# Kernel optimization log

Hardware: AMD Instinct MI355X
Metric: run time of the kernel (lower is better)

## Reference

```python
import jax, jax.numpy as jnp
import numpy as np

D_MODEL = 512
N = 2048
BS = 8


def setup_inputs() -> dict:
    key = jax.random.key(0)
    ks = jax.random.split(key, 5)
    inputs1 = jax.random.normal(ks[0], (BS, N, D_MODEL), dtype=jnp.float32)
    inputs2 = jax.random.normal(ks[1], (BS, N, D_MODEL), dtype=jnp.float32)
    # torch Linear weights: init.normal_(std=0.001), bias=0
    Wq = 0.001 * jax.random.normal(ks[2], (D_MODEL, D_MODEL), dtype=jnp.float32)
    Wk = 0.001 * jax.random.normal(ks[3], (D_MODEL, D_MODEL), dtype=jnp.float32)
    Wv = 0.001 * jax.random.normal(ks[4], (D_MODEL, D_MODEL), dtype=jnp.float32)
    bq = jnp.zeros((D_MODEL,), dtype=jnp.float32)
    bk = jnp.zeros((D_MODEL,), dtype=jnp.float32)
    bv = jnp.zeros((D_MODEL,), dtype=jnp.float32)
    # nn.Parameter(torch.ones((n, n)))
    position_biases = jnp.ones((N, N), dtype=jnp.float32)
    return {"inputs1": inputs1, "inputs2": inputs2, "Wq": Wq, "bq": bq,
            "Wk": Wk, "bk": bk, "Wv": Wv, "bv": bv,
            "position_biases": position_biases}


def reference(inputs1, inputs2, Wq, bq, Wk, bk, Wv, bv, position_biases):
    # torch Linear: y = x @ W.T + b
    q = inputs1 @ Wq.T + bq                     # [b, n, d]
    k = inputs1 @ Wk.T + bk                     # [b, s, d]
    v = inputs2 @ Wv.T + bv                     # [b, s, d]
    # exp(k[b,s,d] + bias[t,s]) = exp(bias)[t,s] * exp(k)[b,s,d] -> separable,
    # avoiding the original's (n, bs, n, dim) broadcast intermediate.
    expB = jnp.exp(position_biases)             # [t, s]
    ek = jnp.exp(k)                             # [b, s, d]
    num = jnp.einsum('ts,bsd->btd', expB, ek * v)
    den = jnp.einsum('ts,bsd->btd', expB, ek)
    return jax.nn.sigmoid(q) * (num / den)      # [b, n, d]
```

## Files before the change

### kernel.cpp

```cpp
#include <hip/hip_runtime.h>

typedef float  f32x4  __attribute__((ext_vector_type(4)));
typedef __bf16 bf16x8 __attribute__((ext_vector_type(8)));
typedef __bf16 bf16x4 __attribute__((ext_vector_type(4)));
typedef __bf16 bf16x2 __attribute__((ext_vector_type(2)));

#define D_MODEL 512
#define SEQ     2048
#define BATCH   8
#define ROWS    (BATCH * SEQ)

#define ASYNC_COPY16(dst_lds, src_glb)                                          \
  __builtin_amdgcn_global_load_lds(                                             \
      (const __attribute__((address_space(1))) void*)(src_glb),                 \
      (__attribute__((address_space(3))) void*)(dst_lds), 16, 0, 0)

__global__ void cvt_x_kernel(const float* __restrict__ in0,
                             const float* __restrict__ in1,
                             __bf16* __restrict__ o0, __bf16* __restrict__ o1,
                             int n4) {
  const float* in = blockIdx.y ? in1 : in0;
  __bf16* out = blockIdx.y ? o1 : o0;
  int i = blockIdx.x * 256 + threadIdx.x;
  if (i >= n4) return;
  float4 v = ((const float4*)in)[i];
  bf16x4 o = { (__bf16)v.x, (__bf16)v.y, (__bf16)v.z, (__bf16)v.w };
  ((bf16x4*)out)[i] = o;
}

__global__ void cvt_w_kernel(const float* __restrict__ Wq,
                             const float* __restrict__ Wk,
                             const float* __restrict__ Wv,
                             const float* __restrict__ bq,
                             const float* __restrict__ bk,
                             __bf16* __restrict__ wqk, __bf16* __restrict__ wvb,
                             float* __restrict__ bqk, int n4) {
  const int y = blockIdx.y;
  const float* in = (y == 0) ? Wq : (y == 1) ? Wk : Wv;
  __bf16* out = (y == 0) ? wqk : (y == 1) ? (wqk + n4 * 4) : wvb;
  int i = blockIdx.x * 256 + threadIdx.x;
  if (y < 2 && blockIdx.x == 0 && threadIdx.x < D_MODEL) {
    int t = threadIdx.x;
    bqk[y * D_MODEL + t] = (y == 0) ? bq[t] : bk[t];
  }
  if (i >= n4) return;
  float4 v = ((const float4*)in)[i];
  bf16x4 o = { (__bf16)v.x, (__bf16)v.y, (__bf16)v.z, (__bf16)v.w };
  ((bf16x4*)out)[i] = o;
}

__global__ void exp_bf16x4_kernel(const float* __restrict__ in,
                                  __bf16* __restrict__ out, int n4) {
  int i = blockIdx.x * 256 + threadIdx.x;
  if (i >= n4) return;
  float4 v = ((const float4*)in)[i];
  bf16x4 o = { (__bf16)__expf(v.x), (__bf16)__expf(v.y),
               (__bf16)__expf(v.z), (__bf16)__expf(v.w) };
  ((bf16x4*)out)[i] = o;
}


template<int DUAL>
__global__ __launch_bounds__(256) void gemm_bk64_kernel(
    const __bf16* __restrict__ A, const __bf16* __restrict__ Bt,
    const float* __restrict__ bias,
    __bf16* __restrict__ out0, __bf16* __restrict__ out1, int K)
{
  __shared__ __align__(16) __bf16 As[128 * 64];
  __shared__ __align__(16) __bf16 Bs[128 * 64];

  const int tid  = threadIdx.x;
  const int wave = tid >> 6;
  const int lane = tid & 63;
  const int quad = lane >> 4;
  const int l16  = lane & 15;
  const int wm   = (wave >> 1) * 64;
  const int wn   = (wave & 1) * 64;
  const int m0 = blockIdx.x * 128;
  const int n0 = blockIdx.y * 128;
  const int l8r = lane >> 3;
  const int scol = ((lane & 7) ^ l8r) * 8;

  const __bf16* ga[4]; const __bf16* gb[4];
  __bf16* la[4]; __bf16* lb[4];
  #pragma unroll
  for (int i = 0; i < 4; ++i) {
    ga[i] = A  + (long long)(m0 + i * 32 + wave * 8 + l8r) * K + scol;
    gb[i] = Bt + (long long)(n0 + i * 32 + wave * 8 + l8r) * K + scol;
    la[i] = As + (i * 32 + wave * 8) * 64;
    lb[i] = Bs + (i * 32 + wave * 8) * 64;
  }

  f32x4 acc[4][4];
  #pragma unroll
  for (int i = 0; i < 4; ++i)
    #pragma unroll
    for (int j = 0; j < 4; ++j) acc[i][j] = (f32x4){0.f, 0.f, 0.f, 0.f};

  for (int k0 = 0; k0 < K; k0 += 64) {
    #pragma unroll
    for (int i = 0; i < 4; ++i) {
      ASYNC_COPY16(la[i], ga[i] + k0);
      ASYNC_COPY16(lb[i], gb[i] + k0);
    }
    __syncthreads();

    #pragma unroll
    for (int kk = 0; kk < 2; ++kk) {
      const int slot = ((quad + kk * 4) ^ (l16 & 7)) * 8;
      bf16x8 af[4], bfr[4];
      #pragma unroll
      for (int i = 0; i < 4; ++i)
        af[i] = *(const bf16x8*)&As[(wm + i * 16 + l16) * 64 + slot];
      #pragma unroll
      for (int j = 0; j < 4; ++j)
        bfr[j] = *(const bf16x8*)&Bs[(wn + j * 16 + l16) * 64 + slot];
      #pragma unroll
      for (int i = 0; i < 4; ++i)
        #pragma unroll
        for (int j = 0; j < 4; ++j)
          acc[i][j] = __builtin_amdgcn_mfma_f32_16x16x32_bf16(af[i], bfr[j],
                                                              acc[i][j], 0, 0, 0);
    }
    __syncthreads();
  }

  #pragma unroll
  for (int j = 0; j < 4; ++j) {
    const int col = n0 + wn + j * 16 + l16;
    const float bv = bias[col];
    #pragma unroll
    for (int i = 0; i < 4; ++i) {
      #pragma unroll
      for (int r = 0; r < 4; ++r) {
        const int row = m0 + wm + i * 16 + quad * 4 + r;
        float x = acc[i][j][r] + bv;
        if (DUAL) {
          if (col < D_MODEL) {
            out0[(long long)row * D_MODEL + col] = (__bf16)(1.f / (1.f + __expf(-x)));
          } else {
            out1[(long long)row * D_MODEL + (col - D_MODEL)] = (__bf16)x;
          }
        } else {
          out0[(long long)row * D_MODEL + col] = (__bf16)x;
        }
      }
    }
  }
}

__global__ __launch_bounds__(256) void einsum_fused_kernel(
    const __bf16* __restrict__ A, const __bf16* __restrict__ BtAll,
    const __bf16* __restrict__ sigq, float* __restrict__ out)
{
  __shared__ __align__(16) __bf16 As[128 * 64];
  __shared__ __align__(16) __bf16 Bs[128 * 64];

  const int b = blockIdx.z;
  const __bf16* Bt = BtAll + (long long)b * (2 * D_MODEL) * SEQ;
  const int K = SEQ;

  const int tid  = threadIdx.x;
  const int wave = tid >> 6;
  const int lane = tid & 63;
  const int quad = lane >> 4;
  const int l16  = lane & 15;
  const int wm   = (wave >> 1) * 64;
  const int wn   = (wave & 1) * 64;
  const int m0 = blockIdx.x * 128;
  const int n0 = blockIdx.y * 128;
  const int l8r = lane >> 3;
  const int scol = ((lane & 7) ^ l8r) * 8;

  const __bf16* ga[4]; const __bf16* gb[4];
  __bf16* la[4]; __bf16* lb[4];
  #pragma unroll
  for (int i = 0; i < 4; ++i) {
    ga[i] = A  + (long long)(m0 + i * 32 + wave * 8 + l8r) * K + scol;
    gb[i] = Bt + (long long)(n0 + i * 32 + wave * 8 + l8r) * K + scol;
    la[i] = As + (i * 32 + wave * 8) * 64;
    lb[i] = Bs + (i * 32 + wave * 8) * 64;
  }

  f32x4 acc[4][4];
  #pragma unroll
  for (int i = 0; i < 4; ++i)
    #pragma unroll
    for (int j = 0; j < 4; ++j) acc[i][j] = (f32x4){0.f, 0.f, 0.f, 0.f};

  for (int k0 = 0; k0 < K; k0 += 64) {
    #pragma unroll
    for (int i = 0; i < 4; ++i) {
      ASYNC_COPY16(la[i], ga[i] + k0);
      ASYNC_COPY16(lb[i], gb[i] + k0);
    }
    __syncthreads();

    #pragma unroll
    for (int kk = 0; kk < 2; ++kk) {
      const int slot = ((quad + kk * 4) ^ (l16 & 7)) * 8;
      bf16x8 af[4], bfr[4];
      #pragma unroll
      for (int i = 0; i < 4; ++i)
        af[i] = *(const bf16x8*)&As[(wm + i * 16 + l16) * 64 + slot];
      #pragma unroll
      for (int j = 0; j < 4; ++j)
        bfr[j] = *(const bf16x8*)&Bs[(wn + j * 16 + l16) * 64 + slot];
      #pragma unroll
      for (int i = 0; i < 4; ++i)
        #pragma unroll
        for (int j = 0; j < 4; ++j)
          acc[i][j] = __builtin_amdgcn_mfma_f32_16x16x32_bf16(af[i], bfr[j],
                                                              acc[i][j], 0, 0, 0);
    }
    __syncthreads();
  }

  const int g = (n0 + wn) >> 6;
  #pragma unroll
  for (int j = 0; j < 2; ++j) {
    const int d = g * 32 + j * 16 + l16;
    #pragma unroll
    for (int i = 0; i < 4; ++i) {
      #pragma unroll
      for (int r = 0; r < 4; ++r) {
        const int row = m0 + wm + i * 16 + quad * 4 + r;
        const long long off = ((long long)b * SEQ + row) * D_MODEL + d;
        const float num = acc[i][j][r];
        const float den = acc[i][j + 2][r];
        out[off] = (float)sigq[off] * (num / den);
      }
    }
  }
}

__global__ __launch_bounds__(256) void transform_transpose_kernel(
    const __bf16* __restrict__ kb, const __bf16* __restrict__ vb,
    __bf16* __restrict__ ekvT)
{
  __shared__ float t_ekv[64][67];
  __shared__ float t_ek[64][67];
  const int b  = blockIdx.z;
  const int s0 = blockIdx.x * 64;
  const int d0 = blockIdx.y * 64;
  const int tx = threadIdx.x;
  const int ty = threadIdx.y;
  const __bf16* kp = kb + (long long)b * SEQ * D_MODEL;
  const __bf16* vp = vb + (long long)b * SEQ * D_MODEL;

  #pragma unroll
  for (int it = 0; it < 8; ++it) {
    const int sl = ty + it * 8;
    const long long base = (long long)(s0 + sl) * D_MODEL + d0 + 2 * tx;
    bf16x2 kk2 = *(const bf16x2*)(kp + base);
    bf16x2 vv2 = *(const bf16x2*)(vp + base);
    float e0 = __expf((float)kk2[0]);
    float e1 = __expf((float)kk2[1]);
    t_ek[sl][2 * tx]      = e0;
    t_ek[sl][2 * tx + 1]  = e1;
    t_ekv[sl][2 * tx]     = e0 * (float)vv2[0];
    t_ekv[sl][2 * tx + 1] = e1 * (float)vv2[1];
  }
  __syncthreads();

  __bf16* outp = ekvT + (long long)b * (2 * D_MODEL) * SEQ;
  #pragma unroll
  for (int it = 0; it < 8; ++it) {
    const int dl = ty + it * 8;
    const int d  = d0 + dl;
    const int gr = (d >> 5) * 64 + (d & 31);
    bf16x2 ev = { (__bf16)t_ekv[2 * tx][dl], (__bf16)t_ekv[2 * tx + 1][dl] };
    bf16x2 ee = { (__bf16)t_ek[2 * tx][dl],  (__bf16)t_ek[2 * tx + 1][dl] };
    *(bf16x2*)(outp + (long long)gr * SEQ + s0 + 2 * tx)        = ev;
    *(bf16x2*)(outp + (long long)(gr + 32) * SEQ + s0 + 2 * tx) = ee;
  }
}

extern "C" void kernel_launch(void* const* d_in, const int* in_sizes, int n_in,
                              void* d_out, int out_size, void* d_ws, size_t ws_size,
                              hipStream_t stream) {
  const float* inputs1 = (const float*)d_in[0];
  const float* inputs2 = (const float*)d_in[1];
  const float* Wq = (const float*)d_in[2];
  const float* bq = (const float*)d_in[3];
  const float* Wk = (const float*)d_in[4];
  const float* bk = (const float*)d_in[5];
  const float* Wv = (const float*)d_in[6];
  const float* bv = (const float*)d_in[7];
  const float* posb = (const float*)d_in[8];
  float* out = (float*)d_out;

  char* ws = (char*)d_ws;
  const long long szX  = (long long)ROWS * D_MODEL * 2;
  const long long szW  = (long long)D_MODEL * D_MODEL * 2;
  const long long szEB = (long long)SEQ * SEQ * 2;
  const long long szT  = (long long)BATCH * 2 * D_MODEL * SEQ * 2;
  __bf16* x1b   = (__bf16*)(ws);                 ws += szX;
  __bf16* x2b   = (__bf16*)(ws);                 ws += szX;
  __bf16* wqk   = (__bf16*)(ws);                 ws += 2 * szW;
  __bf16* wvb   = (__bf16*)(ws);                 ws += szW;
  float*  bqk   = (float*)(ws);                  ws += 2 * D_MODEL * 4;
  __bf16* expBb = (__bf16*)(ws);                 ws += szEB;
  __bf16* sigq  = (__bf16*)(ws);                 ws += szX;
  __bf16* kb2   = (__bf16*)(ws);                 ws += szX;
  __bf16* vb2   = (__bf16*)(ws);                 ws += szX;
  __bf16* ekvT  = (__bf16*)(ws);                 ws += szT;

  const int nX  = ROWS * D_MODEL;
  const int nW  = D_MODEL * D_MODEL;
  const int nEB = SEQ * SEQ;

  {
    dim3 g(nX / 4 / 256, 2, 1);
    cvt_x_kernel<<<g, 256, 0, stream>>>(inputs1, inputs2, x1b, x2b, nX / 4);
  }
  {
    dim3 g(nW / 4 / 256, 3, 1);
    cvt_w_kernel<<<g, 256, 0, stream>>>(Wq, Wk, Wv, bq, bk, wqk, wvb, bqk, nW / 4);
  }
  exp_bf16x4_kernel<<<nEB / 4 / 256, 256, 0, stream>>>(posb, expBb, nEB / 4);

  {
    dim3 gqk(ROWS / 128, (2 * D_MODEL) / 128, 1);
    gemm_bk64_kernel<1><<<gqk, 256, 0, stream>>>(x1b, wqk, bqk, sigq, kb2, D_MODEL);
    dim3 gv(ROWS / 128, D_MODEL / 128, 1);
    gemm_bk64_kernel<0><<<gv, 256, 0, stream>>>(x2b, wvb, bv, vb2, nullptr, D_MODEL);
  }

  {
    dim3 g(SEQ / 64, D_MODEL / 64, BATCH);
    dim3 blk(32, 8, 1);
    transform_transpose_kernel<<<g, blk, 0, stream>>>(kb2, vb2, ekvT);
  }

  {
    dim3 g(SEQ / 128, (2 * D_MODEL) / 128, BATCH);
    einsum_fused_kernel<<<g, 256, 0, stream>>>(expBb, ekvT, sigq, out);
  }
}
```

Measured before the change: 277.1 us.

## Fuse K/V projections with exp-transform and transpose; merge conversion kernels

The three conversion kernels become a single launch. The Q/K/V GEMMs become one projection kernel. Its z=1 half computes K and V tiles together and applies exp(k) and exp(k)*v in the epilogue. It then transposes the result through swizzled LDS straight into the ekvT layout. This removes the separate transform/transpose kernel and the kb/vb round trip through global memory, at the cost of 64KB of LDS and doubled accumulators per block, which may lower occupancy.

```diff
diff --git a/kernel.cpp b/kernel.cpp
--- a/kernel.cpp
+++ b/kernel.cpp
@@ -3,7 +3,6 @@
 typedef float  f32x4  __attribute__((ext_vector_type(4)));
 typedef __bf16 bf16x8 __attribute__((ext_vector_type(8)));
 typedef __bf16 bf16x4 __attribute__((ext_vector_type(4)));
-typedef __bf16 bf16x2 __attribute__((ext_vector_type(2)));
 
 #define D_MODEL 512
 #define SEQ     2048
@@ -15,59 +14,53 @@
       (const __attribute__((address_space(1))) void*)(src_glb),                 \
       (__attribute__((address_space(3))) void*)(dst_lds), 16, 0, 0)
 
-__global__ void cvt_x_kernel(const float* __restrict__ in0,
-                             const float* __restrict__ in1,
-                             __bf16* __restrict__ o0, __bf16* __restrict__ o1,
-                             int n4) {
-  const float* in = blockIdx.y ? in1 : in0;
-  __bf16* out = blockIdx.y ? o1 : o0;
-  int i = blockIdx.x * 256 + threadIdx.x;
-  if (i >= n4) return;
-  float4 v = ((const float4*)in)[i];
-  bf16x4 o = { (__bf16)v.x, (__bf16)v.y, (__bf16)v.z, (__bf16)v.w };
-  ((bf16x4*)out)[i] = o;
+__global__ void cvt_all_kernel(const float* __restrict__ x1,
+                               const float* __restrict__ x2,
+                               const float* __restrict__ posb,
+                               const float* __restrict__ Wq,
+                               const float* __restrict__ Wk,
+                               const float* __restrict__ Wv,
+                               __bf16* __restrict__ x1b, __bf16* __restrict__ x2b,
+                               __bf16* __restrict__ expBb, __bf16* __restrict__ wb)
+{
+  const int y = blockIdx.y;
+  const int i = blockIdx.x * 256 + threadIdx.x;
+  if (y == 0) {
+    float4 v = ((const float4*)x1)[i];
+    bf16x4 o = { (__bf16)v.x, (__bf16)v.y, (__bf16)v.z, (__bf16)v.w };
+    ((bf16x4*)x1b)[i] = o;
+  } else if (y == 1) {
+    float4 v = ((const float4*)x2)[i];
+    bf16x4 o = { (__bf16)v.x, (__bf16)v.y, (__bf16)v.z, (__bf16)v.w };
+    ((bf16x4*)x2b)[i] = o;
+  } else if (y == 2) {
+    if (i < SEQ * SEQ / 4) {
+      float4 v = ((const float4*)posb)[i];
+      bf16x4 o = { (__bf16)__expf(v.x), (__bf16)__expf(v.y),
+                   (__bf16)__expf(v.z), (__bf16)__expf(v.w) };
+      ((bf16x4*)expBb)[i] = o;
+    }
+  } else {
+    const int nW4 = D_MODEL * D_MODEL / 4;
+    if (i < 3 * nW4) {
+      const float* src = (i < nW4) ? Wq : (i < 2 * nW4) ? Wk : Wv;
+      const int ii = i - ((i < nW4) ? 0 : (i < 2 * nW4) ? nW4 : 2 * nW4);
+      float4 v = ((const float4*)src)[ii];
+      bf16x4 o = { (__bf16)v.x, (__bf16)v.y, (__bf16)v.z, (__bf16)v.w };
+      ((bf16x4*)wb)[i] = o;
+    }
+  }
 }
 
-__global__ void cvt_w_kernel(const float* __restrict__ Wq,
-                             const float* __restrict__ Wk,
-                             const float* __restrict__ Wv,
-                             const float* __restrict__ bq,
-                             const float* __restrict__ bk,
-                             __bf16* __restrict__ wqk, __bf16* __restrict__ wvb,
-                             float* __restrict__ bqk, int n4) {
-  const int y = blockIdx.y;
-  const float* in = (y == 0) ? Wq : (y == 1) ? Wk : Wv;
-  __bf16* out = (y == 0) ? wqk : (y == 1) ? (wqk + n4 * 4) : wvb;
-  int i = blockIdx.x * 256 + threadIdx.x;
-  if (y < 2 && blockIdx.x == 0 && threadIdx.x < D_MODEL) {
-    int t = threadIdx.x;
-    bqk[y * D_MODEL + t] = (y == 0) ? bq[t] : bk[t];
-  }
-  if (i >= n4) return;
-  float4 v = ((const float4*)in)[i];
-  bf16x4 o = { (__bf16)v.x, (__bf16)v.y, (__bf16)v.z, (__bf16)v.w };
-  ((bf16x4*)out)[i] = o;
-}
-
-__global__ void exp_bf16x4_kernel(const float* __restrict__ in,
-                                  __bf16* __restrict__ out, int n4) {
-  int i = blockIdx.x * 256 + threadIdx.x;
-  if (i >= n4) return;
-  float4 v = ((const float4*)in)[i];
-  bf16x4 o = { (__bf16)__expf(v.x), (__bf16)__expf(v.y),
-               (__bf16)__expf(v.z), (__bf16)__expf(v.w) };
-  ((bf16x4*)out)[i] = o;
-}
-
-
-template<int DUAL>
-__global__ __launch_bounds__(256) void gemm_bk64_kernel(
-    const __bf16* __restrict__ A, const __bf16* __restrict__ Bt,
-    const float* __restrict__ bias,
-    __bf16* __restrict__ out0, __bf16* __restrict__ out1, int K)
+__global__ __launch_bounds__(256) void proj_kernel(
+    const __bf16* __restrict__ x1b, const __bf16* __restrict__ x2b,
+    const __bf16* __restrict__ wqb, const __bf16* __restrict__ wkb,
+    const __bf16* __restrict__ wvb,
+    const float* __restrict__ bq, const float* __restrict__ bk,
+    const float* __restrict__ bv,
+    __bf16* __restrict__ sigq, __bf16* __restrict__ ekvT)
 {
-  __shared__ __align__(16) __bf16 As[128 * 64];
-  __shared__ __align__(16) __bf16 Bs[128 * 64];
+  __shared__ __align__(16) __bf16 S[4][128 * 64];
 
   const int tid  = threadIdx.x;
   const int wave = tid >> 6;
@@ -80,71 +73,166 @@
   const int n0 = blockIdx.y * 128;
   const int l8r = lane >> 3;
   const int scol = ((lane & 7) ^ l8r) * 8;
-
-  const __bf16* ga[4]; const __bf16* gb[4];
-  __bf16* la[4]; __bf16* lb[4];
-  #pragma unroll
-  for (int i = 0; i < 4; ++i) {
-    ga[i] = A  + (long long)(m0 + i * 32 + wave * 8 + l8r) * K + scol;
-    gb[i] = Bt + (long long)(n0 + i * 32 + wave * 8 + l8r) * K + scol;
-    la[i] = As + (i * 32 + wave * 8) * 64;
-    lb[i] = Bs + (i * 32 + wave * 8) * 64;
-  }
-
-  f32x4 acc[4][4];
-  #pragma unroll
-  for (int i = 0; i < 4; ++i)
-    #pragma unroll
-    for (int j = 0; j < 4; ++j) acc[i][j] = (f32x4){0.f, 0.f, 0.f, 0.f};
-
-  for (int k0 = 0; k0 < K; k0 += 64) {
+  const int K = D_MODEL;
+
+  if (blockIdx.z == 0) {
+    __bf16* As = S[0];
+    __bf16* Bs = S[1];
+    const __bf16* ga[4]; const __bf16* gb[4];
+    __bf16* la[4]; __bf16* lb[4];
     #pragma unroll
     for (int i = 0; i < 4; ++i) {
-      ASYNC_COPY16(la[i], ga[i] + k0);
-      ASYNC_COPY16(lb[i], gb[i] + k0);
+      ga[i] = x1b + (long long)(m0 + i * 32 + wave * 8 + l8r) * K + scol;
+      gb[i] = wqb + (long long)(n0 + i * 32 + wave * 8 + l8r) * K + scol;
+      la[i] = As + (i * 32 + wave * 8) * 64;
+      lb[i] = Bs + (i * 32 + wave * 8) * 64;
+    }
+    f32x4 acc[4][4];
+    #pragma unroll
+    for (int i = 0; i < 4; ++i)
+      #pragma unroll
+      for (int j = 0; j < 4; ++j) acc[i][j] = (f32x4){0.f, 0.f, 0.f, 0.f};
+
+    for (int k0 = 0; k0 < K; k0 += 64) {
+      #pragma unroll
+      for (int i = 0; i < 4; ++i) {
+        ASYNC_COPY16(la[i], ga[i] + k0);
+        ASYNC_COPY16(lb[i], gb[i] + k0);
+      }
+      __syncthreads();
+      #pragma unroll
+      for (int kk = 0; kk < 2; ++kk) {
+        const int slot = ((quad + kk * 4) ^ (l16 & 7)) * 8;
+        bf16x8 af[4], bfr[4];
+        #pragma unroll
+        for (int i = 0; i < 4; ++i)
+          af[i] = *(const bf16x8*)&As[(wm + i * 16 + l16) * 64 + slot];
+        #pragma unroll
+        for (int j = 0; j < 4; ++j)
+          bfr[j] = *(const bf16x8*)&Bs[(wn + j * 16 + l16) * 64 + slot];
+        #pragma unroll
+        for (int i = 0; i < 4; ++i)
+          #pragma unroll
+          for (int j = 0; j < 4; ++j)
+            acc[i][j] = __builtin_amdgcn_mfma_f32_16x16x32_bf16(af[i], bfr[j],
+                                                                acc[i][j], 0, 0, 0);
+      }
+      __syncthreads();
+    }
+    #pragma unroll
+    for (int j = 0; j < 4; ++j) {
+      const int col = n0 + wn + j * 16 + l16;
+      const float bqv = bq[col];
+      #pragma unroll
+      for (int i = 0; i < 4; ++i)
+        #pragma unroll
+        for (int r = 0; r < 4; ++r) {
+          const int row = m0 + wm + i * 16 + quad * 4 + r;
+          float x = acc[i][j][r] + bqv;
+          sigq[(long long)row * D_MODEL + col] = (__bf16)(1.f / (1.f + __expf(-x)));
+        }
+    }
+  } else {
+    __bf16* A1s = S[0];
+    __bf16* A2s = S[1];
+    __bf16* Bks = S[2];
+    __bf16* Bvs = S[3];
+    const __bf16* ga1[4]; const __bf16* ga2[4];
+    const __bf16* gbk[4]; const __bf16* gbv[4];
+    #pragma unroll
+    for (int i = 0; i < 4; ++i) {
+      const long long roff = (long long)(i * 32 + wave * 8 + l8r);
+      ga1[i] = x1b + (m0 + roff) * K + scol;
+      ga2[i] = x2b + (m0 + roff) * K + scol;
+      gbk[i] = wkb + (n0 + roff) * K + scol;
+      gbv[i] = wvb + (n0 + roff) * K + scol;
+    }
+    f32x4 acck[4][4], accv[4][4];
+    #pragma unroll
+    for (int i = 0; i < 4; ++i)
+      #pragma unroll
+      for (int j = 0; j < 4; ++j) {
+        acck[i][j] = (f32x4){0.f, 0.f, 0.f, 0.f};
+        accv[i][j] = (f32x4){0.f, 0.f, 0.f, 0.f};
+      }
+
+    for (int k0 = 0; k0 < K; k0 += 64) {
+      #pragma unroll
+      for (int i = 0; i < 4; ++i) {
+        const int lo = (i * 32 + wave * 8) * 64;
+        ASYNC_COPY16(A1s + lo, ga1[i] + k0);
+        ASYNC_COPY16(A2s + lo, ga2[i] + k0);
+        ASYNC_COPY16(Bks + lo, gbk[i] + k0);
+        ASYNC_COPY16(Bvs + lo, gbv[i] + k0);
+      }
+      __syncthreads();
+      #pragma unroll
+      for (int kk = 0; kk < 2; ++kk) {
+        const int slot = ((quad + kk * 4) ^ (l16 & 7)) * 8;
+        bf16x8 af[4], bfr[4];
+        #pragma unroll
+        for (int i = 0; i < 4; ++i)
+          af[i] = *(const bf16x8*)&A1s[(wm + i * 16 + l16) * 64 + slot];
+        #pragma unroll
+        for (int j = 0; j < 4; ++j)
+          bfr[j] = *(const bf16x8*)&Bks[(wn + j * 16 + l16) * 64 + slot];
+        #pragma unroll
+        for (int i = 0; i < 4; ++i)
+          #pragma unroll
+          for (int j = 0; j < 4; ++j)
+            acck[i][j] = __builtin_amdgcn_mfma_f32_16x16x32_bf16(af[i], bfr[j],
+                                                                 acck[i][j], 0, 0, 0);
+        #pragma unroll
+        for (int i = 0; i < 4; ++i)
+          af[i] = *(const bf16x8*)&A2s[(wm + i * 16 + l16) * 64 + slot];
+        #pragma unroll
+        for (int j = 0; j < 4; ++j)
+          bfr[j] = *(const bf16x8*)&Bvs[(wn + j * 16 + l16) * 64 + slot];
+        #pragma unroll
+        for (int i = 0; i < 4; ++i)
+          #pragma unroll
+          for (int j = 0; j < 4; ++j)
+            accv[i][j] = __builtin_amdgcn_mfma_f32_16x16x32_bf16(af[i], bfr[j],
+                                                                 accv[i][j], 0, 0, 0);
+      }
+      __syncthreads();
+    }
+
+    __bf16* L = &S[0][0];
+    #pragma unroll
+    for (int j = 0; j < 4; ++j) {
+      const int col = wn + j * 16 + l16;
+      const float bkv = bk[n0 + col];
+      const float bvv = bv[n0 + col];
+      const int Rekv = (col >> 5) * 64 + (col & 31);
+      const int Rek  = Rekv + 32;
+      #pragma unroll
+      for (int i = 0; i < 4; ++i) {
+        const int sb = wm + i * 16 + quad * 4;
+        bf16x4 pk, pv;
+        #pragma unroll
+        for (int r = 0; r < 4; ++r) {
+          const float ek = __expf(acck[i][j][r] + bkv);
+          const float vv = accv[i][j][r] + bvv;
+          pk[r] = (__bf16)ek;
+          pv[r] = (__bf16)(ek * vv);
+        }
+        const int c = sb >> 3, w8 = sb & 7;
+        *(bf16x4*)&L[Rekv * 128 + (((c) ^ (Rekv & 15)) << 3) + w8] = pv;
+        *(bf16x4*)&L[Rek  * 128 + (((c) ^ (Rek  & 15)) << 3) + w8] = pk;
+      }
     }
     __syncthreads();
 
-    #pragma unroll
-    for (int kk = 0; kk < 2; ++kk) {
-      const int slot = ((quad + kk * 4) ^ (l16 & 7)) * 8;
-      bf16x8 af[4], bfr[4];
-      #pragma unroll
-      for (int i = 0; i < 4; ++i)
-        af[i] = *(const bf16x8*)&As[(wm + i * 16 + l16) * 64 + slot];
-      #pragma unroll
-      for (int j = 0; j < 4; ++j)
-        bfr[j] = *(const bf16x8*)&Bs[(wn + j * 16 + l16) * 64 + slot];
-      #pragma unroll
-      for (int i = 0; i < 4; ++i)
-        #pragma unroll
-        for (int j = 0; j < 4; ++j)
-          acc[i][j] = __builtin_amdgcn_mfma_f32_16x16x32_bf16(af[i], bfr[j],
-                                                              acc[i][j], 0, 0, 0);
-    }
-    __syncthreads();
-  }
-
-  #pragma unroll
-  for (int j = 0; j < 4; ++j) {
-    const int col = n0 + wn + j * 16 + l16;
-    const float bv = bias[col];
-    #pragma unroll
-    for (int i = 0; i < 4; ++i) {
-      #pragma unroll
-      for (int r = 0; r < 4; ++r) {
-        const int row = m0 + wm + i * 16 + quad * 4 + r;
-        float x = acc[i][j][r] + bv;
-        if (DUAL) {
-          if (col < D_MODEL) {
-            out0[(long long)row * D_MODEL + col] = (__bf16)(1.f / (1.f + __expf(-x)));
-          } else {
-            out1[(long long)row * D_MODEL + (col - D_MODEL)] = (__bf16)x;
-          }
-        } else {
-          out0[(long long)row * D_MODEL + col] = (__bf16)x;
-        }
-      }
+    const long long obase = (long long)(m0 >> 11) * (2 * D_MODEL) * SEQ
+                          + (long long)(m0 & (SEQ - 1));
+    #pragma unroll
+    for (int ii = 0; ii < 16; ++ii) {
+      const int flat = ii * 256 + tid;
+      const int R = flat >> 4;
+      const int c = flat & 15;
+      bf16x8 vv = *(const bf16x8*)&L[R * 128 + ((c ^ (R & 15)) << 3)];
+      *(bf16x8*)(ekvT + obase + (long long)(blockIdx.y * 256 + R) * SEQ + c * 8) = vv;
     }
   }
 }
@@ -231,48 +319,6 @@
         out[off] = (float)sigq[off] * (num / den);
       }
     }
-  }
-}
-
-__global__ __launch_bounds__(256) void transform_transpose_kernel(
-    const __bf16* __restrict__ kb, const __bf16* __restrict__ vb,
-    __bf16* __restrict__ ekvT)
-{
-  __shared__ float t_ekv[64][67];
-  __shared__ float t_ek[64][67];
-  const int b  = blockIdx.z;
-  const int s0 = blockIdx.x * 64;
-  const int d0 = blockIdx.y * 64;
-  const int tx = threadIdx.x;
-  const int ty = threadIdx.y;
-  const __bf16* kp = kb + (long long)b * SEQ * D_MODEL;
-  const __bf16* vp = vb + (long long)b * SEQ * D_MODEL;
-
-  #pragma unroll
-  for (int it = 0; it < 8; ++it) {
-    const int sl = ty + it * 8;
-    const long long base = (long long)(s0 + sl) * D_MODEL + d0 + 2 * tx;
-    bf16x2 kk2 = *(const bf16x2*)(kp + base);
-    bf16x2 vv2 = *(const bf16x2*)(vp + base);
-    float e0 = __expf((float)kk2[0]);
-    float e1 = __expf((float)kk2[1]);
-    t_ek[sl][2 * tx]      = e0;
-    t_ek[sl][2 * tx + 1]  = e1;
-    t_ekv[sl][2 * tx]     = e0 * (float)vv2[0];
-    t_ekv[sl][2 * tx + 1] = e1 * (float)vv2[1];
-  }
-  __syncthreads();
-
-  __bf16* outp = ekvT + (long long)b * (2 * D_MODEL) * SEQ;
-  #pragma unroll
-  for (int it = 0; it < 8; ++it) {
-    const int dl = ty + it * 8;
-    const int d  = d0 + dl;
-    const int gr = (d >> 5) * 64 + (d & 31);
-    bf16x2 ev = { (__bf16)t_ekv[2 * tx][dl], (__bf16)t_ekv[2 * tx + 1][dl] };
-    bf16x2 ee = { (__bf16)t_ek[2 * tx][dl],  (__bf16)t_ek[2 * tx + 1][dl] };
-    *(bf16x2*)(outp + (long long)gr * SEQ + s0 + 2 * tx)        = ev;
-    *(bf16x2*)(outp + (long long)(gr + 32) * SEQ + s0 + 2 * tx) = ee;
   }
 }
 
@@ -297,40 +343,26 @@
   const long long szT  = (long long)BATCH * 2 * D_MODEL * SEQ * 2;
   __bf16* x1b   = (__bf16*)(ws);                 ws += szX;
   __bf16* x2b   = (__bf16*)(ws);                 ws += szX;
-  __bf16* wqk   = (__bf16*)(ws);                 ws += 2 * szW;
-  __bf16* wvb   = (__bf16*)(ws);                 ws += szW;
-  float*  bqk   = (float*)(ws);                  ws += 2 * D_MODEL * 4;
+  __bf16* wb    = (__bf16*)(ws);                 ws += 3 * szW;
   __bf16* expBb = (__bf16*)(ws);                 ws += szEB;
   __bf16* sigq  = (__bf16*)(ws);                 ws += szX;
-  __bf16* kb2   = (__bf16*)(ws);                 ws += szX;
-  __bf16* vb2   = (__bf16*)(ws);                 ws += szX;
   __bf16* ekvT  = (__bf16*)(ws);                 ws += szT;
-
-  const int nX  = ROWS * D_MODEL;
-  const int nW  = D_MODEL * D_MODEL;
-  const int nEB = SEQ * SEQ;
+  __bf16* wqb = wb;
+  __bf16* wkb = wb + (long long)D_MODEL * D_MODEL;
+  __bf16* wvb = wb + 2LL * D_MODEL * D_MODEL;
+
+  const int nX = ROWS * D_MODEL;
 
   {
-    dim3 g(nX / 4 / 256, 2, 1);
-    cvt_x_kernel<<<g, 256, 0, stream>>>(inputs1, inputs2, x1b, x2b, nX / 4);
-  }
+    dim3 g(nX / 4 / 256, 4, 1);
+    cvt_all_kernel<<<g, 256, 0, stream>>>(inputs1, inputs2, posb, Wq, Wk, Wv,
+                                          x1b, x2b, expBb, wb);
+  }
+
   {
-    dim3 g(nW / 4 / 256, 3, 1);
-    cvt_w_kernel<<<g, 256, 0, stream>>>(Wq, Wk, Wv, bq, bk, wqk, wvb, bqk, nW / 4);
-  }
-  exp_bf16x4_kernel<<<nEB / 4 / 256, 256, 0, stream>>>(posb, expBb, nEB / 4);
-
-  {
-    dim3 gqk(ROWS / 128, (2 * D_MODEL) / 128, 1);
-    gemm_bk64_kernel<1><<<gqk, 256, 0, stream>>>(x1b, wqk, bqk, sigq, kb2, D_MODEL);
-    dim3 gv(ROWS / 128, D_MODEL / 128, 1);
-    gemm_bk64_kernel<0><<<gv, 256, 0, stream>>>(x2b, wvb, bv, vb2, nullptr, D_MODEL);
-  }
-
-  {
-    dim3 g(SEQ / 64, D_MODEL / 64, BATCH);
-    dim3 blk(32, 8, 1);
-    transform_transpose_kernel<<<g, blk, 0, stream>>>(kb2, vb2, ekvT);
+    dim3 g(ROWS / 128, D_MODEL / 128, 2);
+    proj_kernel<<<g, 256, 0, stream>>>(x1b, x2b, wqb, wkb, wvb,
+                                       bq, bk, bv, sigq, ekvT);
   }
 
   {
```

Result: no change. 273.1 us (-1.4%).
